# Kernel optimization log

Hardware: AMD Instinct MI355X
Metric: run time of the kernel (lower is better)

## Reference

```python
import jax, jax.numpy as jnp
import numpy as np

B, S, DIM = 2, 2048, 2048
H, KVH, HD = 16, 4, 128
WIN = 512
ROPE_BASE = 10000.0
EPS = 1.1920928955078125e-07  # torch F.rms_norm default eps for fp32


def setup_inputs() -> dict:
    key = jax.random.key(0)
    ks = jax.random.split(key, 6)
    kv_dim = KVH * HD
    sc = lambda fan_in: 1.0 / np.sqrt(fan_in)
    return {
        "x": jax.random.normal(ks[0], (B, S, DIM), jnp.float32),
        "Wq": jax.random.normal(ks[1], (DIM, DIM), jnp.float32) * sc(DIM),
        "Wk": jax.random.normal(ks[2], (kv_dim, DIM), jnp.float32) * sc(DIM),
        "Wv": jax.random.normal(ks[3], (kv_dim, DIM), jnp.float32) * sc(DIM),
        "Wo": jax.random.normal(ks[4], (DIM, DIM), jnp.float32) * sc(DIM),
        "q_gain": jnp.ones((H,), jnp.float32),
    }


def _rms_norm(x):
    return x * jax.lax.rsqrt(jnp.mean(x * x, axis=-1, keepdims=True) + EPS)


def _rope_tables(seqlen, dtype):
    half = HD // 2
    inv_freq = ROPE_BASE ** (-jnp.arange(0, half, dtype=jnp.float32) / half)
    freqs = jnp.arange(seqlen, dtype=jnp.float32)[:, None] * inv_freq[None, :]  # [S, HD/2]
    return jnp.cos(freqs).astype(dtype), jnp.sin(freqs).astype(dtype)


def _apply_rotary(x, cos, sin):
    # x: [B, H, S, HD]; cos/sin: [S, HD/2]
    half = x.shape[-1] // 2
    x1, x2 = x[..., :half], x[..., half:]
    c = cos[None, None, :, :]
    s = sin[None, None, :, :]
    return jnp.concatenate([x1 * c + x2 * s, -x1 * s + x2 * c], axis=-1)


def reference(x, Wq, Wk, Wv, Wo, q_gain):
    bsz, seqlen, dim = x.shape
    q = jnp.einsum("bsd,ed->bse", x, Wq).reshape(bsz, seqlen, H, HD).transpose(0, 2, 1, 3)
    k = jnp.einsum("bsd,ed->bse", x, Wk).reshape(bsz, seqlen, KVH, HD).transpose(0, 2, 1, 3)
    v = jnp.einsum("bsd,ed->bse", x, Wv).reshape(bsz, seqlen, KVH, HD).transpose(0, 2, 1, 3)

    q = _rms_norm(q)
    k = _rms_norm(k)

    cos, sin = _rope_tables(seqlen, q.dtype)
    q = _apply_rotary(q, cos, sin)
    k = _apply_rotary(k, cos, sin)

    q = q * q_gain[None, :, None, None]

    # GQA: expand kv heads to match query heads
    rep = H // KVH
    k = jnp.repeat(k, rep, axis=1)
    v = jnp.repeat(v, rep, axis=1)

    row = jnp.arange(seqlen)[:, None]
    col = jnp.arange(seqlen)[None, :]
    mask = (col <= row) & (col >= row - WIN + 1)  # [S, S]

    scale = 1.0 / np.sqrt(HD)
    scores = jnp.einsum("bhsd,bhtd->bhst", q, k) * scale
    scores = jnp.where(mask[None, None, :, :], scores, -jnp.inf)
    attn = jax.nn.softmax(scores, axis=-1)
    y = jnp.einsum("bhst,bhtd->bhsd", attn, v)  # [B, H, S, HD]

    y = y.transpose(0, 2, 1, 3).reshape(bsz, seqlen, dim)
    return jnp.einsum("bsd,ed->bse", y, Wo)
```

## Files before the change

### kernel.cpp

```cpp
#include <hip/hip_runtime.h>

#define S_LEN 2048
#define DIM   2048
#define NH    16
#define NKV   4
#define HD    128
#define WIN   512
#define BATCH 2

typedef __bf16 bf16x8 __attribute__((ext_vector_type(8)));
typedef __bf16 bf16x4 __attribute__((ext_vector_type(4)));
typedef float  f32x4  __attribute__((ext_vector_type(4)));

union U8 { bf16x8 v; bf16x4 h[2]; };

__device__ inline void async_load16(const void* g, void* l) {
  __builtin_amdgcn_global_load_lds(
      (const __attribute__((address_space(1))) unsigned int*)g,
      (__attribute__((address_space(3))) unsigned int*)l, 16, 0, 0);
}

__global__ __launch_bounds__(256) void preprocess_kernel(
    const float* __restrict__ x,
    const float* __restrict__ Wq, const float* __restrict__ Wk,
    const float* __restrict__ Wv, const float* __restrict__ Wo,
    __bf16* __restrict__ xb, __bf16* __restrict__ wqkv, __bf16* __restrict__ wob,
    float* __restrict__ cosT, float* __restrict__ sinT) {
  const int blk = blockIdx.x, tid = threadIdx.x;
  if (blk < 8192) {
    int i = blk * 256 + tid;
    float4 v = ((const float4*)x)[i];
    bf16x4 o;
    o[0] = (__bf16)v.x; o[1] = (__bf16)v.y; o[2] = (__bf16)v.z; o[3] = (__bf16)v.w;
    ((bf16x4*)xb)[i] = o;
  } else if (blk < 18432) {
    int i = (blk - 8192) * 256 + tid;
    int orow = i >> 9, c = i & 511;
    const float* src;
    __bf16* dst;
    long soff;
    if (orow < 2048) {
      int n = orow & 127;
      int sr = (orow & ~127) + ((n >> 5) << 4) + (n & 15) + (((n >> 4) & 1) << 6);
      src = Wq; soff = (long)sr * 512 + c; dst = wqkv + (long)orow * 2048;
    } else if (orow < 2560) {
      int lr = orow - 2048, n = lr & 127;
      int sr = (lr & ~127) + ((n >> 5) << 4) + (n & 15) + (((n >> 4) & 1) << 6);
      src = Wk; soff = (long)sr * 512 + c; dst = wqkv + (long)orow * 2048;
    } else if (orow < 3072) {
      src = Wv; soff = (long)(orow - 2560) * 512 + c; dst = wqkv + (long)orow * 2048;
    } else {
      src = Wo; soff = (long)(orow - 3072) * 512 + c; dst = wob + (long)(orow - 3072) * 2048;
    }
    float4 v = ((const float4*)src)[soff];
    bf16x4 o;
    o[0] = (__bf16)v.x; o[1] = (__bf16)v.y; o[2] = (__bf16)v.z; o[3] = (__bf16)v.w;
    ((bf16x4*)dst)[c] = o;
  } else {
    int idx = (blk - 18432) * 256 + tid;
    int s = idx >> 6, d = idx & 63;
    float f = (float)s * powf(10000.f, -(float)d * (1.f / 64.f));
    float sn, cs;
    sincosf(f, &sn, &cs);
    cosT[idx] = cs;
    sinT[idx] = sn;
  }
}

__global__ __launch_bounds__(256) void gemm_bt(
    const __bf16* __restrict__ A, const __bf16* __restrict__ Bt,
    float* __restrict__ C, int M, int N, int K) {
  __shared__ __bf16 As[128 * 32];
  __shared__ __bf16 Bs[128 * 32];
  const int t = threadIdx.x;
  const int wid = t >> 6, lane = t & 63;
  const int quad = lane >> 4, l15 = lane & 15;
  const long m0 = (long)blockIdx.x * 128, n0 = (long)blockIdx.y * 128;
  const int wm = (wid >> 1) * 64, wn = (wid & 1) * 64;

  const __bf16* ga = A + (m0 + (t >> 2)) * (long)K + (t & 3) * 8;
  const __bf16* gb = Bt + (n0 + (t >> 2)) * (long)K + (t & 3) * 8;
  char* lA = (char*)As + wid * 1024;
  char* lB = (char*)Bs + wid * 1024;
  const long rstride = 64L * K;

  f32x4 zero = {0.f, 0.f, 0.f, 0.f};
  f32x4 acc[4][4];
#pragma unroll
  for (int i = 0; i < 4; ++i)
#pragma unroll
    for (int j = 0; j < 4; ++j) acc[i][j] = zero;

  for (int k0 = 0; k0 < K; k0 += 32) {
    async_load16(ga + k0, lA);
    async_load16(ga + k0 + rstride, lA + 4096);
    async_load16(gb + k0, lB);
    async_load16(gb + k0 + rstride, lB + 4096);
    __syncthreads();
    bf16x8 af[4], bfr[4];
#pragma unroll
    for (int i = 0; i < 4; ++i) {
      af[i] = *(const bf16x8*)(As + (wm + i * 16 + l15) * 32 + quad * 8);
      bfr[i] = *(const bf16x8*)(Bs + (wn + i * 16 + l15) * 32 + quad * 8);
    }
#pragma unroll
    for (int i = 0; i < 4; ++i)
#pragma unroll
      for (int j = 0; j < 4; ++j)
        acc[i][j] = __builtin_amdgcn_mfma_f32_16x16x32_bf16(af[i], bfr[j], acc[i][j], 0, 0, 0);
    __syncthreads();
  }

#pragma unroll
  for (int i = 0; i < 4; ++i)
#pragma unroll
    for (int j = 0; j < 4; ++j)
#pragma unroll
      for (int r = 0; r < 4; ++r)
        C[(m0 + wm + i * 16 + quad * 4 + r) * (long)N + n0 + wn + j * 16 + l15] = acc[i][j][r];
}

__global__ __launch_bounds__(256) void gemm_qkv(
    const __bf16* __restrict__ A, const __bf16* __restrict__ Bt,
    const float* __restrict__ gain,
    const float* __restrict__ cosT, const float* __restrict__ sinT,
    __bf16* __restrict__ Qo, __bf16* __restrict__ Ko, __bf16* __restrict__ Vt) {
  __shared__ __bf16 As[128 * 32];
  __shared__ __bf16 Bs[128 * 32];
  const int K = 2048;
  const int t = threadIdx.x;
  const int wid = t >> 6, lane = t & 63;
  const int quad = lane >> 4, l15 = lane & 15;
  const long m0 = (long)blockIdx.x * 128, n0 = (long)blockIdx.y * 128;
  const int wm = (wid >> 1) * 64, wn = (wid & 1) * 64;

  const __bf16* ga = A + (m0 + (t >> 2)) * (long)K + (t & 3) * 8;
  const __bf16* gb = Bt + (n0 + (t >> 2)) * (long)K + (t & 3) * 8;
  char* lA = (char*)As + wid * 1024;
  char* lB = (char*)Bs + wid * 1024;
  const long rstride = 64L * K;

  f32x4 zero = {0.f, 0.f, 0.f, 0.f};
  f32x4 acc[4][4];
#pragma unroll
  for (int i = 0; i < 4; ++i)
#pragma unroll
    for (int j = 0; j < 4; ++j) acc[i][j] = zero;

  for (int k0 = 0; k0 < K; k0 += 32) {
    async_load16(ga + k0, lA);
    async_load16(ga + k0 + rstride, lA + 4096);
    async_load16(gb + k0, lB);
    async_load16(gb + k0 + rstride, lB + 4096);
    __syncthreads();
    bf16x8 af[4], bfr[4];
#pragma unroll
    for (int i = 0; i < 4; ++i) {
      af[i] = *(const bf16x8*)(As + (wm + i * 16 + l15) * 32 + quad * 8);
      bfr[i] = *(const bf16x8*)(Bs + (wn + i * 16 + l15) * 32 + quad * 8);
    }
#pragma unroll
    for (int i = 0; i < 4; ++i)
#pragma unroll
      for (int j = 0; j < 4; ++j)
        acc[i][j] = __builtin_amdgcn_mfma_f32_16x16x32_bf16(af[i], bfr[j], acc[i][j], 0, 0, 0);
    __syncthreads();
  }

  const int by = blockIdx.y;
  const int srow0 = (int)(m0 & 2047);
  const int bb = (int)(m0 >> 11);

  if (by >= 20) {
    const int kvh = by - 20;
    __bf16* Vb = Vt + ((long)(bb * NKV + kvh)) * HD * S_LEN;
#pragma unroll
    for (int i = 0; i < 4; ++i)
#pragma unroll
      for (int j = 0; j < 4; ++j) {
        int d = wn + j * 16 + l15;
        int s0 = srow0 + wm + i * 16 + quad * 4;
        bf16x4 o;
#pragma unroll
        for (int r = 0; r < 4; ++r) o[r] = (__bf16)acc[i][j][r];
        *(bf16x4*)(Vb + (long)d * S_LEN + s0) = o;
      }
  } else {
    float* sums = (float*)As;
#pragma unroll
    for (int i = 0; i < 4; ++i)
#pragma unroll
      for (int r = 0; r < 4; ++r) {
        float t2 = acc[i][0][r] * acc[i][0][r] + acc[i][1][r] * acc[i][1][r] +
                   acc[i][2][r] * acc[i][2][r] + acc[i][3][r] * acc[i][3][r];
#pragma unroll
        for (int off = 1; off < 16; off <<= 1) t2 += __shfl_xor(t2, off, 64);
        if (l15 == 0) sums[(wm + i * 16 + quad * 4 + r) * 2 + (wn >> 6)] = t2;
      }
    __syncthreads();

    float g;
    __bf16* base;
    if (by < 16) {
      g = gain[by] * 0.08838834764831845f;
      base = Qo + ((long)(bb * NH + by)) * S_LEN * HD;
    } else {
      g = 1.f;
      base = Ko + ((long)(bb * NKV + (by - 16))) * S_LEN * HD;
    }
#pragma unroll
    for (int i = 0; i < 4; ++i)
#pragma unroll
      for (int r = 0; r < 4; ++r) {
        int lrow = wm + i * 16 + quad * 4 + r;
        int srow = srow0 + lrow;
        float rs = rsqrtf((sums[lrow * 2] + sums[lrow * 2 + 1]) * (1.f / 128.f) +
                          1.1920928955078125e-07f);
#pragma unroll
        for (int a = 0; a < 2; ++a) {
          int dlow = (wn >> 1) + a * 16 + l15;
          float cv = cosT[srow * 64 + dlow];
          float sv = sinT[srow * 64 + dlow];
          float x1 = acc[i][2 * a][r] * rs;
          float x2 = acc[i][2 * a + 1][r] * rs;
          base[(long)srow * HD + wn + (2 * a) * 16 + l15] = (__bf16)((x1 * cv + x2 * sv) * g);
          base[(long)srow * HD + wn + (2 * a + 1) * 16 + l15] = (__bf16)((-x1 * sv + x2 * cv) * g);
        }
      }
  }
}

__global__ __launch_bounds__(128, 1) void attn_kernel(
    const __bf16* __restrict__ Q,
    const __bf16* __restrict__ K,
    const __bf16* __restrict__ Vt,
    const float* __restrict__ gain,
    __bf16* __restrict__ Y) {
  __shared__ __bf16 Ks[64 * 128];
  __shared__ __bf16 Vs[128 * 64];
  __shared__ __bf16 Ps[2][64 * 64];
  __shared__ float  Ls[2][64];

  const int t = threadIdx.x;
  const int wid = t >> 6, lane = t & 63;
  const int quad = lane >> 4, l15 = lane & 15;
  const int qt_blk = 15 - blockIdx.x;
  const int h = blockIdx.y, b = blockIdx.z;
  const int kv = h >> 2;
  const int t0 = qt_blk * 128;
  const int r0 = t0 + wid * 64;

  const __bf16* Qb = Q + ((long)(b * NH + h)) * S_LEN * HD;
  const __bf16* Kb = K + ((long)(b * NKV + kv)) * S_LEN * HD;
  const __bf16* Vb = Vt + ((long)(b * NKV + kv)) * HD * S_LEN;
  const float M = 11.3137085f * fabsf(gain[h]);

  bf16x8 qf[4][4];
#pragma unroll
  for (int qt = 0; qt < 4; ++qt)
#pragma unroll
    for (int c = 0; c < 4; ++c)
      qf[qt][c] = *(const bf16x8*)(Qb + (long)(r0 + qt * 16 + l15) * HD + c * 32 + quad * 8);

  f32x4 zero = {0.f, 0.f, 0.f, 0.f};
  f32x4 acc[4][8];
#pragma unroll
  for (int mt = 0; mt < 4; ++mt)
#pragma unroll
    for (int d = 0; d < 8; ++d) acc[mt][d] = zero;
  float lac[4] = {0.f, 0.f, 0.f, 0.f};

  int ksrc[8], vsrc[8];
#pragma unroll
  for (int j = 0; j < 8; ++j) {
    int kr = j * 8 + (t >> 4);
    ksrc[j] = kr * HD + (((t & 15) ^ (kr & 15)) << 3);
    int vd = j * 16 + (t >> 3);
    vsrc[j] = vd * S_LEN + (((t & 7) ^ (vd & 7)) << 3);
  }

  const int kstart = (t0 >= WIN) ? (t0 - WIN) : 0;
  const int ntiles = (t0 + 128 - kstart) >> 6;

  for (int it = 0; it < ntiles; ++it) {
    const int kt = kstart + it * 64;
#pragma unroll
    for (int j = 0; j < 8; ++j) {
      async_load16(Kb + (long)kt * HD + ksrc[j], (char*)Ks + j * 2048 + t * 16);
      async_load16(Vb + kt + vsrc[j], (char*)Vs + j * 2048 + t * 16);
    }
    __syncthreads();

    if (kt <= r0 + 63 && kt + 63 >= r0 - (WIN - 1)) {
#pragma unroll
      for (int kti = 0; kti < 4; ++kti) {
        bf16x8 kf[4];
#pragma unroll
        for (int c = 0; c < 4; ++c)
          kf[c] = *(const bf16x8*)(Ks + (kti * 16 + l15) * 128 +
                                   ((((c << 2) + quad) ^ l15) << 3));
#pragma unroll
        for (int qt = 0; qt < 4; ++qt) {
          f32x4 sc = zero;
#pragma unroll
          for (int c = 0; c < 4; ++c)
            sc = __builtin_amdgcn_mfma_f32_16x16x32_bf16(kf[c], qf[qt][c], sc, 0, 0, 0);
          const int q = qt * 16 + l15;
          const int qg = r0 + q;
          const int kbase = kt + kti * 16 + quad * 4;
          bf16x4 pv;
#pragma unroll
          for (int r = 0; r < 4; ++r) {
            int key = kbase + r;
            float p = (key <= qg && key >= qg - (WIN - 1)) ? __expf(sc[r] - M) : 0.f;
            lac[qt] += p;
            pv[r] = (__bf16)p;
          }
          const int cb = kti * 4 + quad;
          *(bf16x4*)(&Ps[wid][q * 64 + ((cb ^ l15) << 2)]) = pv;
        }
      }
      bf16x8 pf[4][2];
#pragma unroll
      for (int mt = 0; mt < 4; ++mt)
#pragma unroll
        for (int kc = 0; kc < 2; ++kc) {
          const int q = mt * 16 + l15;
          U8 u;
          u.h[0] = *(const bf16x4*)(&Ps[wid][q * 64 + (((kc * 8 + quad * 2) ^ l15) << 2)]);
          u.h[1] = *(const bf16x4*)(&Ps[wid][q * 64 + (((kc * 8 + quad * 2 + 1) ^ l15) << 2)]);
          pf[mt][kc] = u.v;
        }
#pragma unroll
      for (int dt = 0; dt < 8; ++dt)
#pragma unroll
        for (int kc = 0; kc < 2; ++kc) {
          bf16x8 vf = *(const bf16x8*)(Vs + (dt * 16 + l15) * 64 +
                                       ((((kc << 2) + quad) ^ (l15 & 7)) << 3));
#pragma unroll
          for (int mt = 0; mt < 4; ++mt)
            acc[mt][dt] = __builtin_amdgcn_mfma_f32_16x16x32_bf16(pf[mt][kc], vf, acc[mt][dt], 0, 0, 0);
        }
    }
    __syncthreads();
  }

#pragma unroll
  for (int qt = 0; qt < 4; ++qt) {
    float s = lac[qt];
    s += __shfl_xor(s, 16, 64);
    s += __shfl_xor(s, 32, 64);
    if (quad == 0) Ls[wid][qt * 16 + l15] = s;
  }
  __bf16* Yb = Y + ((long)b * S_LEN) * DIM + h * HD;
#pragma unroll
  for (int mt = 0; mt < 4; ++mt)
#pragma unroll
    for (int r = 0; r < 4; ++r) {
      float il = 1.f / Ls[wid][mt * 16 + quad * 4 + r];
      const long row = r0 + mt * 16 + quad * 4 + r;
#pragma unroll
      for (int dt = 0; dt < 8; ++dt)
        Yb[row * DIM + dt * 16 + l15] = (__bf16)(acc[mt][dt][r] * il);
    }
}

extern "C" void kernel_launch(void* const* d_in, const int* in_sizes, int n_in,
                              void* d_out, int out_size, void* d_ws, size_t ws_size,
                              hipStream_t stream) {
  (void)in_sizes; (void)n_in; (void)out_size; (void)ws_size;
  const float* x  = (const float*)d_in[0];
  const float* Wq = (const float*)d_in[1];
  const float* Wk = (const float*)d_in[2];
  const float* Wv = (const float*)d_in[3];
  const float* Wo = (const float*)d_in[4];
  const float* qg = (const float*)d_in[5];
  float* out = (float*)d_out;

  char* ws = (char*)d_ws;
  size_t off = 0;
  auto alloc = [&](size_t bytes) -> void* {
    void* p = ws + off;
    off += (bytes + 255) & ~(size_t)255;
    return p;
  };
  __bf16* xb   = (__bf16*)alloc(8388608ull * 2);
  __bf16* wqkv = (__bf16*)alloc(3072ull * 2048 * 2);
  __bf16* wob  = (__bf16*)alloc(2048ull * 2048 * 2);
  __bf16* qo   = (__bf16*)alloc((size_t)BATCH * NH * S_LEN * HD * 2);
  __bf16* ko   = (__bf16*)alloc((size_t)BATCH * NKV * S_LEN * HD * 2);
  __bf16* vt   = (__bf16*)alloc((size_t)BATCH * NKV * HD * S_LEN * 2);
  float*  cosT = (float*)alloc(2048ull * 64 * 4);
  float*  sinT = (float*)alloc(2048ull * 64 * 4);
  __bf16* yb   = xb;

  preprocess_kernel<<<18944, 256, 0, stream>>>(x, Wq, Wk, Wv, Wo, xb, wqkv, wob,
                                               cosT, sinT);
  gemm_qkv<<<dim3(32, 24), 256, 0, stream>>>(xb, wqkv, qg, cosT, sinT, qo, ko, vt);
  attn_kernel<<<dim3(16, 16, 2), 128, 0, stream>>>(qo, ko, vt, qg, yb);
  gemm_bt<<<dim3(32, 16), 256, 0, stream>>>(yb, wob, out, 4096, 2048, 2048);
}
```

Baseline: 272.3 us.

## Restructure attention blocks to 4 waves of 16 query rows each

The attention kernel now uses 256-thread blocks, where each of the 4 waves handles 16 query rows instead of 64. A block covers 64 query rows, so the grid doubles to 32 tiles per head. Per-wave registers (Q fragments, accumulators, row sums) shrink by about 4x, which allows launch_bounds(256,4) and much higher occupancy. It also removes the LDS row-sum buffer in favour of shuffles. The trade-off is less reuse of each K/V tile per query row and more blocks reloading overlapping K/V windows.

```diff
diff --git a/kernel.cpp b/kernel.cpp
--- a/kernel.cpp
+++ b/kernel.cpp
@@ -230,7 +230,7 @@
   }
 }
 
-__global__ __launch_bounds__(128, 1) void attn_kernel(
+__global__ __launch_bounds__(256, 4) void attn_kernel(
     const __bf16* __restrict__ Q,
     const __bf16* __restrict__ K,
     const __bf16* __restrict__ Vt,
@@ -238,60 +238,55 @@
     __bf16* __restrict__ Y) {
   __shared__ __bf16 Ks[64 * 128];
   __shared__ __bf16 Vs[128 * 64];
-  __shared__ __bf16 Ps[2][64 * 64];
-  __shared__ float  Ls[2][64];
+  __shared__ __bf16 Ps[4][16 * 64];
 
   const int t = threadIdx.x;
   const int wid = t >> 6, lane = t & 63;
   const int quad = lane >> 4, l15 = lane & 15;
-  const int qt_blk = 15 - blockIdx.x;
+  const int qt_blk = 31 - blockIdx.x;
   const int h = blockIdx.y, b = blockIdx.z;
   const int kv = h >> 2;
-  const int t0 = qt_blk * 128;
-  const int r0 = t0 + wid * 64;
+  const int t0 = qt_blk * 64;
+  const int r0 = t0 + wid * 16;
 
   const __bf16* Qb = Q + ((long)(b * NH + h)) * S_LEN * HD;
   const __bf16* Kb = K + ((long)(b * NKV + kv)) * S_LEN * HD;
   const __bf16* Vb = Vt + ((long)(b * NKV + kv)) * HD * S_LEN;
   const float M = 11.3137085f * fabsf(gain[h]);
 
-  bf16x8 qf[4][4];
-#pragma unroll
-  for (int qt = 0; qt < 4; ++qt)
-#pragma unroll
-    for (int c = 0; c < 4; ++c)
-      qf[qt][c] = *(const bf16x8*)(Qb + (long)(r0 + qt * 16 + l15) * HD + c * 32 + quad * 8);
+  bf16x8 qf[4];
+#pragma unroll
+  for (int c = 0; c < 4; ++c)
+    qf[c] = *(const bf16x8*)(Qb + (long)(r0 + l15) * HD + c * 32 + quad * 8);
 
   f32x4 zero = {0.f, 0.f, 0.f, 0.f};
-  f32x4 acc[4][8];
-#pragma unroll
-  for (int mt = 0; mt < 4; ++mt)
-#pragma unroll
-    for (int d = 0; d < 8; ++d) acc[mt][d] = zero;
-  float lac[4] = {0.f, 0.f, 0.f, 0.f};
-
-  int ksrc[8], vsrc[8];
-#pragma unroll
-  for (int j = 0; j < 8; ++j) {
-    int kr = j * 8 + (t >> 4);
+  f32x4 acc[8];
+#pragma unroll
+  for (int d = 0; d < 8; ++d) acc[d] = zero;
+  float lac = 0.f;
+
+  int ksrc[4], vsrc[4];
+#pragma unroll
+  for (int j = 0; j < 4; ++j) {
+    int kr = j * 16 + (t >> 4);
     ksrc[j] = kr * HD + (((t & 15) ^ (kr & 15)) << 3);
-    int vd = j * 16 + (t >> 3);
+    int vd = j * 32 + (t >> 3);
     vsrc[j] = vd * S_LEN + (((t & 7) ^ (vd & 7)) << 3);
   }
 
   const int kstart = (t0 >= WIN) ? (t0 - WIN) : 0;
-  const int ntiles = (t0 + 128 - kstart) >> 6;
+  const int ntiles = (t0 + 64 - kstart) >> 6;
 
   for (int it = 0; it < ntiles; ++it) {
     const int kt = kstart + it * 64;
 #pragma unroll
-    for (int j = 0; j < 8; ++j) {
-      async_load16(Kb + (long)kt * HD + ksrc[j], (char*)Ks + j * 2048 + t * 16);
-      async_load16(Vb + kt + vsrc[j], (char*)Vs + j * 2048 + t * 16);
-    }
-    __syncthreads();
-
-    if (kt <= r0 + 63 && kt + 63 >= r0 - (WIN - 1)) {
+    for (int j = 0; j < 4; ++j) {
+      async_load16(Kb + (long)kt * HD + ksrc[j], (char*)Ks + j * 4096 + t * 16);
+      async_load16(Vb + kt + vsrc[j], (char*)Vs + j * 4096 + t * 16);
+    }
+    __syncthreads();
+
+    if (kt <= r0 + 15 && kt + 63 >= r0 - (WIN - 1)) {
 #pragma unroll
       for (int kti = 0; kti < 4; ++kti) {
         bf16x8 kf[4];
@@ -299,70 +294,55 @@
         for (int c = 0; c < 4; ++c)
           kf[c] = *(const bf16x8*)(Ks + (kti * 16 + l15) * 128 +
                                    ((((c << 2) + quad) ^ l15) << 3));
-#pragma unroll
-        for (int qt = 0; qt < 4; ++qt) {
-          f32x4 sc = zero;
-#pragma unroll
-          for (int c = 0; c < 4; ++c)
-            sc = __builtin_amdgcn_mfma_f32_16x16x32_bf16(kf[c], qf[qt][c], sc, 0, 0, 0);
-          const int q = qt * 16 + l15;
-          const int qg = r0 + q;
-          const int kbase = kt + kti * 16 + quad * 4;
-          bf16x4 pv;
-#pragma unroll
-          for (int r = 0; r < 4; ++r) {
-            int key = kbase + r;
-            float p = (key <= qg && key >= qg - (WIN - 1)) ? __expf(sc[r] - M) : 0.f;
-            lac[qt] += p;
-            pv[r] = (__bf16)p;
-          }
-          const int cb = kti * 4 + quad;
-          *(bf16x4*)(&Ps[wid][q * 64 + ((cb ^ l15) << 2)]) = pv;
+        f32x4 sc = zero;
+#pragma unroll
+        for (int c = 0; c < 4; ++c)
+          sc = __builtin_amdgcn_mfma_f32_16x16x32_bf16(kf[c], qf[c], sc, 0, 0, 0);
+        const int qg = r0 + l15;
+        const int kbase = kt + kti * 16 + quad * 4;
+        bf16x4 pv;
+#pragma unroll
+        for (int r = 0; r < 4; ++r) {
+          int key = kbase + r;
+          float p = (key <= qg && key >= qg - (WIN - 1)) ? __expf(sc[r] - M) : 0.f;
+          lac += p;
+          pv[r] = (__bf16)p;
         }
-      }
-      bf16x8 pf[4][2];
-#pragma unroll
-      for (int mt = 0; mt < 4; ++mt)
-#pragma unroll
-        for (int kc = 0; kc < 2; ++kc) {
-          const int q = mt * 16 + l15;
-          U8 u;
-          u.h[0] = *(const bf16x4*)(&Ps[wid][q * 64 + (((kc * 8 + quad * 2) ^ l15) << 2)]);
-          u.h[1] = *(const bf16x4*)(&Ps[wid][q * 64 + (((kc * 8 + quad * 2 + 1) ^ l15) << 2)]);
-          pf[mt][kc] = u.v;
-        }
+        const int cb = kti * 4 + quad;
+        *(bf16x4*)(&Ps[wid][l15 * 64 + ((cb ^ l15) << 2)]) = pv;
+      }
+      bf16x8 pf[2];
+#pragma unroll
+      for (int kc = 0; kc < 2; ++kc) {
+        U8 u;
+        u.h[0] = *(const bf16x4*)(&Ps[wid][l15 * 64 + (((kc * 8 + quad * 2) ^ l15) << 2)]);
+        u.h[1] = *(const bf16x4*)(&Ps[wid][l15 * 64 + (((kc * 8 + quad * 2 + 1) ^ l15) << 2)]);
+        pf[kc] = u.v;
+      }
 #pragma unroll
       for (int dt = 0; dt < 8; ++dt)
 #pragma unroll
         for (int kc = 0; kc < 2; ++kc) {
           bf16x8 vf = *(const bf16x8*)(Vs + (dt * 16 + l15) * 64 +
                                        ((((kc << 2) + quad) ^ (l15 & 7)) << 3));
-#pragma unroll
-          for (int mt = 0; mt < 4; ++mt)
-            acc[mt][dt] = __builtin_amdgcn_mfma_f32_16x16x32_bf16(pf[mt][kc], vf, acc[mt][dt], 0, 0, 0);
+          acc[dt] = __builtin_amdgcn_mfma_f32_16x16x32_bf16(pf[kc], vf, acc[dt], 0, 0, 0);
         }
     }
     __syncthreads();
   }
 
-#pragma unroll
-  for (int qt = 0; qt < 4; ++qt) {
-    float s = lac[qt];
-    s += __shfl_xor(s, 16, 64);
-    s += __shfl_xor(s, 32, 64);
-    if (quad == 0) Ls[wid][qt * 16 + l15] = s;
-  }
+  float s = lac;
+  s += __shfl_xor(s, 16, 64);
+  s += __shfl_xor(s, 32, 64);
   __bf16* Yb = Y + ((long)b * S_LEN) * DIM + h * HD;
 #pragma unroll
-  for (int mt = 0; mt < 4; ++mt)
-#pragma unroll
-    for (int r = 0; r < 4; ++r) {
-      float il = 1.f / Ls[wid][mt * 16 + quad * 4 + r];
-      const long row = r0 + mt * 16 + quad * 4 + r;
-#pragma unroll
-      for (int dt = 0; dt < 8; ++dt)
-        Yb[row * DIM + dt * 16 + l15] = (__bf16)(acc[mt][dt][r] * il);
-    }
+  for (int r = 0; r < 4; ++r) {
+    const int row = quad * 4 + r;
+    float il = 1.f / __shfl(s, row, 64);
+#pragma unroll
+    for (int dt = 0; dt < 8; ++dt)
+      Yb[(long)(r0 + row) * DIM + dt * 16 + l15] = (__bf16)(acc[dt][r] * il);
+  }
 }
 
 extern "C" void kernel_launch(void* const* d_in, const int* in_sizes, int n_in,
@@ -397,6 +377,6 @@
   preprocess_kernel<<<18944, 256, 0, stream>>>(x, Wq, Wk, Wv, Wo, xb, wqkv, wob,
                                                cosT, sinT);
   gemm_qkv<<<dim3(32, 24), 256, 0, stream>>>(xb, wqkv, qg, cosT, sinT, qo, ko, vt);
-  attn_kernel<<<dim3(16, 16, 2), 128, 0, stream>>>(qo, ko, vt, qg, yb);
+  attn_kernel<<<dim3(32, 16, 2), 256, 0, stream>>>(qo, ko, vt, qg, yb);
   gemm_bt<<<dim3(32, 16), 256, 0, stream>>>(yb, wob, out, 4096, 2048, 2048);
 }
```

New measurement: 262.1 us. -3.8%, faster.
